# Performance work log

Measured on AMD Instinct MI355X. Metric: run time of the kernel, lower is better.

The kernel has to match this reference:

```python
import jax, jax.numpy as jnp
import numpy as np

EMBED_DIM = 32
DELTA_V = 0.5
DELTA_D = 3.0
NUM_LABELS = 20  # instance labels are 1..NUM_LABELS; 0 is background


def _safe_sqrt(x):
    # sqrt with zero-safe gradient (matches norm of identical points -> 0)
    s = jnp.where(x > 0, x, 1.0)
    return jnp.where(x > 0, jnp.sqrt(s), 0.0)


def _per_batch(emb, seg):
    # emb: [D, N], seg: [N] int labels in 0..L (0 = background)
    D, N = emb.shape
    L = NUM_LABELS
    dt = emb.dtype
    ones = jnp.ones((N,), dt)
    counts = jax.ops.segment_sum(ones, seg, num_segments=L + 1)          # [L+1]
    sums = jax.ops.segment_sum(emb.T, seg, num_segments=L + 1)          # [L+1, D]
    means = sums / jnp.maximum(counts, 1.0)[:, None]                     # [L+1, D]
    present = (counts > 0).at[0].set(False)                              # [L+1]
    num_lanes = jnp.sum(present.astype(dt))

    # --- variance (pull) loss: each pixel vs its own instance centroid ---
    mpix = means[seg]                                                    # [N, D] gather
    sq = jnp.sum((emb.T - mpix) ** 2, axis=1)                            # [N]
    d = _safe_sqrt(sq)
    v = jnp.maximum(d - DELTA_V, 0.0) ** 2 * (seg > 0).astype(dt)        # background excluded
    vsum = jax.ops.segment_sum(v, seg, num_segments=L + 1)               # [L+1]
    vmean = vsum / jnp.maximum(counts, 1.0)
    var_loss = jnp.sum(vmean * present.astype(dt)) / jnp.maximum(num_lanes, 1.0)
    var_loss = jnp.where(num_lanes > 0, var_loss, jnp.zeros((), dt))

    # --- distance (push) loss between present centroids ---
    m = means[1:]                                                        # [L, D]
    p = present[1:]                                                      # [L]
    sqd = jnp.sum((m[:, None, :] - m[None, :, :]) ** 2, axis=-1)         # [L, L]
    dist = _safe_sqrt(sqd)
    pair = (p[:, None] & p[None, :]) & ~jnp.eye(L, dtype=bool)
    dl = jnp.sum(jnp.maximum(DELTA_D - dist, 0.0) ** 2 * pair.astype(dt))
    denom = jnp.maximum(num_lanes * (num_lanes - 1.0), 1.0)
    dist_loss = jnp.where(num_lanes > 1, dl / denom / 2.0, jnp.zeros((), dt))
    return var_loss, dist_loss


def setup_inputs() -> dict:
    key = jax.random.key(0)
    k1, k2 = jax.random.split(key)
    B, D, N = 8, EMBED_DIM, 65536  # 256x256 BEV raster flattened
    embedding = jax.random.normal(k1, (B, D, N), dtype=jnp.float32)
    seg_gt = jax.random.randint(k2, (B, N), 0, NUM_LABELS + 1, dtype=jnp.int32)
    return {"embedding": embedding, "seg_gt": seg_gt}


def reference(embedding, seg_gt):
    var_b, dist_b = jax.vmap(_per_batch)(embedding, seg_gt)  # [B], [B]
    var_loss = jnp.mean(var_b)
    dist_loss = jnp.mean(dist_b)
    reg_loss = jnp.zeros((), embedding.dtype)
    return (var_loss, dist_loss, reg_loss)
```

## Files before the change

### kernel.cpp

```cpp
#include <hip/hip_runtime.h>
#include <hip/hip_cooperative_groups.h>
namespace cg = cooperative_groups;

#define NSEG 21
#define NLBL 20
#define DIM  32
#define NS   64
#define NREP 16
#define DV   0.5f
#define DD   3.0f
#define BATCH 8
#define N_PIX 65536
#define SMS  36
#define TILE_B 65536
#define SEGT_B 1024
#define DYNB  (TILE_B + SEGT_B)

using short8 = __attribute__((ext_vector_type(8))) short;
using f32x4  = __attribute__((ext_vector_type(4))) float;

#define P_OFF  0
#define C2_OFF (BATCH*DIM*NLBL*NS)
#define M_OFF  (C2_OFF + BATCH*NLBL*NS)
#define CN_OFF (M_OFF + BATCH*NLBL*DIM)
#define VS_OFF (CN_OFF + BATCH*NLBL)
#define BAR_OFF (VS_OFF + 8*BATCH*NLBL)
#define V_OFF  (BAR_OFF + 8)
#define PB_OFF (V_OFF + BATCH*NLBL*NS)

__device__ __forceinline__ short bf16rne(float f) {
  const unsigned u = __builtin_bit_cast(unsigned, f);
  return (short)((u + 0x7FFFu + ((u >> 16) & 1u)) >> 16);
}

__device__ __forceinline__ void momentsBody(const float* __restrict__ emb,
                                            const int* __restrict__ seg,
                                            float* __restrict__ ws,
                                            float* lred, ushort* tile,
                                            unsigned char* segt,
                                            int bx, int b, int tid) {
  const int wv = tid >> 6, lane = tid & 63;
  const int lr = lane & 15, lg = lane >> 4;
  const float* rowA0 = emb + ((size_t)b * DIM + lr) * N_PIX;
  const float* rowA1 = rowA0 + (size_t)16 * N_PIX;
  const int*   segb  = seg + (size_t)b * N_PIX;

  f32x4 s00 = {0,0,0,0}, s01 = {0,0,0,0}, s10 = {0,0,0,0}, s11 = {0,0,0,0};
  f32x4 c0  = {0,0,0,0}, c1  = {0,0,0,0};
  short8 ones;
  #pragma unroll
  for (int j = 0; j < 8; ++j) ones[j] = (short)0x3F80;

  #pragma unroll 2
  for (int t = 0; t < 8; ++t) {
    const int kl = wv * 256 + t * 32 + lg * 8;
    const int koff = bx * 1024 + kl;
    const float4 a00 = *(const float4*)(rowA0 + koff);
    const float4 a01 = *(const float4*)(rowA0 + koff + 4);
    const float4 a10 = *(const float4*)(rowA1 + koff);
    const float4 a11 = *(const float4*)(rowA1 + koff + 4);
    const int4   g0  = *(const int4*)(segb + koff);
    const int4   g1  = *(const int4*)(segb + koff + 4);

    short8 fa0, fa1, fb0, fb1;
    fa0[0] = bf16rne(a00.x); fa0[1] = bf16rne(a00.y);
    fa0[2] = bf16rne(a00.z); fa0[3] = bf16rne(a00.w);
    fa0[4] = bf16rne(a01.x); fa0[5] = bf16rne(a01.y);
    fa0[6] = bf16rne(a01.z); fa0[7] = bf16rne(a01.w);
    fa1[0] = bf16rne(a10.x); fa1[1] = bf16rne(a10.y);
    fa1[2] = bf16rne(a10.z); fa1[3] = bf16rne(a10.w);
    fa1[4] = bf16rne(a11.x); fa1[5] = bf16rne(a11.y);
    fa1[6] = bf16rne(a11.z); fa1[7] = bf16rne(a11.w);
    const int lab0 = lr + 1, lab1 = lr + 17;
    fb0[0] = (g0.x == lab0) ? (short)0x3F80 : (short)0;
    fb0[1] = (g0.y == lab0) ? (short)0x3F80 : (short)0;
    fb0[2] = (g0.z == lab0) ? (short)0x3F80 : (short)0;
    fb0[3] = (g0.w == lab0) ? (short)0x3F80 : (short)0;
    fb0[4] = (g1.x == lab0) ? (short)0x3F80 : (short)0;
    fb0[5] = (g1.y == lab0) ? (short)0x3F80 : (short)0;
    fb0[6] = (g1.z == lab0) ? (short)0x3F80 : (short)0;
    fb0[7] = (g1.w == lab0) ? (short)0x3F80 : (short)0;
    fb1[0] = (g0.x == lab1) ? (short)0x3F80 : (short)0;
    fb1[1] = (g0.y == lab1) ? (short)0x3F80 : (short)0;
    fb1[2] = (g0.z == lab1) ? (short)0x3F80 : (short)0;
    fb1[3] = (g0.w == lab1) ? (short)0x3F80 : (short)0;
    fb1[4] = (g1.x == lab1) ? (short)0x3F80 : (short)0;
    fb1[5] = (g1.y == lab1) ? (short)0x3F80 : (short)0;
    fb1[6] = (g1.z == lab1) ? (short)0x3F80 : (short)0;
    fb1[7] = (g1.w == lab1) ? (short)0x3F80 : (short)0;

    const int o = kl >> 3, om = o & 7;
    *(short8*)&tile[o * 256 + ((lr ^ om) << 3)] = fa0;
    *(short8*)&tile[o * 256 + (((lr ^ om) + 16) << 3)] = fa1;
    if (lr == 0) {
      unsigned long long pk =
          (unsigned long long)(g0.x & 255)        | ((unsigned long long)(g0.y & 255) << 8) |
          ((unsigned long long)(g0.z & 255) << 16) | ((unsigned long long)(g0.w & 255) << 24) |
          ((unsigned long long)(g1.x & 255) << 32) | ((unsigned long long)(g1.y & 255) << 40) |
          ((unsigned long long)(g1.z & 255) << 48) | ((unsigned long long)(g1.w & 255) << 56);
      *(unsigned long long*)&segt[o * 8] = pk;
    }

    s00 = __builtin_amdgcn_mfma_f32_16x16x32_bf16(fa0, fb0, s00, 0, 0, 0);
    s01 = __builtin_amdgcn_mfma_f32_16x16x32_bf16(fa0, fb1, s01, 0, 0, 0);
    s10 = __builtin_amdgcn_mfma_f32_16x16x32_bf16(fa1, fb0, s10, 0, 0, 0);
    s11 = __builtin_amdgcn_mfma_f32_16x16x32_bf16(fa1, fb1, s11, 0, 0, 0);
    c0  = __builtin_amdgcn_mfma_f32_16x16x32_bf16(ones, fb0, c0, 0, 0, 0);
    c1  = __builtin_amdgcn_mfma_f32_16x16x32_bf16(ones, fb1, c1, 0, 0, 0);
  }

  float vals[24];
  #pragma unroll
  for (int r = 0; r < 4; ++r) {
    vals[0 * 4 + r] = s00[r]; vals[1 * 4 + r] = s01[r];
    vals[2 * 4 + r] = s10[r]; vals[3 * 4 + r] = s11[r];
    vals[4 * 4 + r] = c0[r];  vals[5 * 4 + r] = c1[r];
  }
  #pragma unroll
  for (int w = 0; w < 4; ++w) {
    if (wv == w) {
      float* base = lred + lane * 4;
      if (w == 0) {
        #pragma unroll
        for (int f = 0; f < 6; ++f)
          #pragma unroll
          for (int r = 0; r < 4; ++r) base[f * 256 + r] = vals[f * 4 + r];
      } else {
        #pragma unroll
        for (int f = 0; f < 6; ++f)
          #pragma unroll
          for (int r = 0; r < 4; ++r) base[f * 256 + r] += vals[f * 4 + r];
      }
    }
    __syncthreads();
  }
  for (int i = tid; i < 1536; i += 256) {
    const float v = lred[i];
    const int f = i >> 8, ln = (i >> 2) & 63, r = i & 3;
    const int col = ln & 15, row = ((ln >> 4) << 2) | r;
    if (f < 4) {
      const int d = (f >> 1) * 16 + row;
      const int lcol = (f & 1) * 16 + col;
      if (lcol < NLBL)
        ws[P_OFF + (((size_t)(b * DIM + d) * NLBL) + lcol) * NS + bx] = v;
    } else {
      const int lcol = (f & 1) * 16 + col;
      if (row == 0 && lcol < NLBL)
        ws[C2_OFF + ((size_t)b * NLBL + lcol) * NS + bx] = v;
    }
  }
}

__device__ __forceinline__ void meansBody(float* __restrict__ ws, float* s_c,
                                          int bx8, int b, int tid) {
  if (tid < NLBL) {
    const float4* cp = (const float4*)(ws + C2_OFF + ((size_t)b * NLBL + tid) * NS);
    float q0 = 0.f, q1 = 0.f, q2 = 0.f, q3 = 0.f;
    #pragma unroll
    for (int k = 0; k < NS / 4; k += 4) {
      const float4 v0 = cp[k], v1 = cp[k + 1], v2 = cp[k + 2], v3 = cp[k + 3];
      q0 += v0.x + v0.y + v0.z + v0.w;
      q1 += v1.x + v1.y + v1.z + v1.w;
      q2 += v2.x + v2.y + v2.z + v2.w;
      q3 += v3.x + v3.y + v3.z + v3.w;
    }
    const float c = q0 + q1 + q2 + q3;
    if (bx8 == 0) ws[CN_OFF + b * NLBL + tid] = c;
    s_c[tid] = fmaxf(c, 1.f);
  }
  __syncthreads();
  if (tid < 80) {
    const int m = bx8 * 80 + tid;
    const int l = m >> 5, d = m & 31;
    const float4* pp = (const float4*)(ws + P_OFF + (((size_t)(b * DIM + d) * NLBL) + l) * NS);
    float q0 = 0.f, q1 = 0.f, q2 = 0.f, q3 = 0.f;
    #pragma unroll
    for (int k = 0; k < NS / 4; k += 4) {
      const float4 v0 = pp[k], v1 = pp[k + 1], v2 = pp[k + 2], v3 = pp[k + 3];
      q0 += v0.x + v0.y + v0.z + v0.w;
      q1 += v1.x + v1.y + v1.z + v1.w;
      q2 += v2.x + v2.y + v2.z + v2.w;
      q3 += v3.x + v3.y + v3.z + v3.w;
    }
    ws[M_OFF + (size_t)b * NLBL * DIM + m] = (q0 + q1 + q2 + q3) / s_c[l];
  }
}

__device__ __forceinline__ void loadMeans(const float* __restrict__ ws,
                                          float* s_m, int b, int tid) {
  for (int i = tid; i < NSEG * SMS; i += 256) s_m[i] = 0.f;
  __syncthreads();
  if (tid < 160) {
    const float4 v = ((const float4*)(ws + M_OFF + (size_t)b * NLBL * DIM))[tid];
    const int flat = tid * 4, l = flat >> 5, d = flat & 31;
    float* dst = &s_m[(l + 1) * SMS + d];
    dst[0] = v.x; dst[1] = v.y; dst[2] = v.z; dst[3] = v.w;
  }
}

__device__ __forceinline__ void varTileCompute(const ushort* tile,
                                               const unsigned char* segt,
                                               const float* s_m, float* s_v,
                                               int tid) {
  const int px0 = tid * 4;
  const int o = px0 >> 3, om = o & 7, p8 = px0 & 7;
  const int la0 = segt[px0], la1 = segt[px0 + 1], la2 = segt[px0 + 2], la3 = segt[px0 + 3];
  float q0 = 0.f, q1 = 0.f, q2 = 0.f, q3 = 0.f;
  #pragma unroll
  for (int db = 0; db < 8; ++db) {
    const f32x4 m0 = *(const f32x4*)&s_m[la0 * SMS + db * 4];
    const f32x4 m1 = *(const f32x4*)&s_m[la1 * SMS + db * 4];
    const f32x4 m2 = *(const f32x4*)&s_m[la2 * SMS + db * 4];
    const f32x4 m3 = *(const f32x4*)&s_m[la3 * SMS + db * 4];
    #pragma unroll
    for (int dd = 0; dd < 4; ++dd) {
      const int d = db * 4 + dd;
      const ushort4 ev = *(const ushort4*)&tile[o * 256 + ((d ^ om) << 3) + p8];
      float t;
      t = __builtin_bit_cast(float, (unsigned)ev.x << 16) - m0[dd]; q0 += t * t;
      t = __builtin_bit_cast(float, (unsigned)ev.y << 16) - m1[dd]; q1 += t * t;
      t = __builtin_bit_cast(float, (unsigned)ev.z << 16) - m2[dd]; q2 += t * t;
      t = __builtin_bit_cast(float, (unsigned)ev.w << 16) - m3[dd]; q3 += t * t;
    }
  }
  const int rb = (tid & (NREP - 1)) * NSEG;
  if (la0 > 0) { const float r = sqrtf(q0) - DV; if (r > 0.f) atomicAdd(&s_v[rb + la0], r * r); }
  if (la1 > 0) { const float r = sqrtf(q1) - DV; if (r > 0.f) atomicAdd(&s_v[rb + la1], r * r); }
  if (la2 > 0) { const float r = sqrtf(q2) - DV; if (r > 0.f) atomicAdd(&s_v[rb + la2], r * r); }
  if (la3 > 0) { const float r = sqrtf(q3) - DV; if (r > 0.f) atomicAdd(&s_v[rb + la3], r * r); }
}

__global__ __launch_bounds__(256, 2)
void k_fused(const float* __restrict__ emb, const int* __restrict__ seg,
             float* __restrict__ ws, float* __restrict__ out) {
  extern __shared__ __align__(16) char dynls[];
  ushort* tile = (ushort*)dynls;
  unsigned char* segt = (unsigned char*)(dynls + TILE_B);
  __shared__ __align__(16) float lred[1536];
  __shared__ __align__(16) float s_m[NSEG * SMS];
  __shared__ float s_v[NREP * NSEG];
  __shared__ float s_c[NLBL];
  __shared__ float s_vs[NLBL];
  __shared__ int   s_p[NLBL];
  __shared__ float s_red[4];
  __shared__ int   s_last;
  cg::grid_group gg = cg::this_grid();
  const int tid = threadIdx.x, bx = blockIdx.x, b = blockIdx.y;
  const int wv = tid >> 6, lane = tid & 63;

  if (bx < 8 && tid < NLBL)
    ws[VS_OFF + ((size_t)bx * BATCH + b) * NLBL + tid] = 0.f;
  if (bx == 8 && tid == 0) ((unsigned*)(ws + BAR_OFF))[b] = 0u;
  if (bx == 9 && b == 0 && tid < 3) out[tid] = 0.f;

  momentsBody(emb, seg, ws, lred, tile, segt, bx, b, tid);
  gg.sync();

  if (bx < 8) meansBody(ws, s_c, bx, b, tid);
  gg.sync();

  for (int i = tid; i < NREP * NSEG; i += 256) s_v[i] = 0.f;
  loadMeans(ws, s_m, b, tid);
  __syncthreads();
  varTileCompute(tile, segt, s_m, s_v, tid);
  __syncthreads();
  if (tid < NLBL) {
    float v = 0.f;
    #pragma unroll
    for (int r = 0; r < NREP; ++r) v += s_v[r * NSEG + (tid + 1)];
    atomicAdd(&ws[VS_OFF + ((size_t)(bx & 7) * BATCH + b) * NLBL + tid], v);
  }
  __syncthreads();
  if (tid == 0) {
    __threadfence();
    unsigned* ctr = (unsigned*)(ws + BAR_OFF);
    s_last = (atomicAdd(&ctr[b], 1u) == NS - 1) ? 1 : 0;
  }
  __syncthreads();

  if (s_last) {
    __threadfence();
    if (tid < 160) {
      const int g = tid >> 3, j = tid & 7;
      float s = atomicAdd(&ws[VS_OFF + ((size_t)j * BATCH + b) * NLBL + g], 0.f);
      s += __shfl_xor(s, 1, 64); s += __shfl_xor(s, 2, 64); s += __shfl_xor(s, 4, 64);
      if (j == 0) s_vs[g] = s;
    }
    if (tid < NLBL) {
      const float c = ws[CN_OFF + b * NLBL + tid];
      s_c[tid] = c;
      s_p[tid] = (c > 0.f) ? 1 : 0;
    }
    __syncthreads();
    float dl = 0.f;
    for (int p = tid; p < NLBL * NLBL; p += 256) {
      const int i = p / NLBL, j = p - (p / NLBL) * NLBL;
      if (i != j && s_p[i] && s_p[j]) {
        float sq = 0.f;
        #pragma unroll
        for (int d = 0; d < DIM; ++d) {
          const float t = s_m[(i + 1) * SMS + d] - s_m[(j + 1) * SMS + d];
          sq += t * t;
        }
        const float r = DD - sqrtf(sq);
        if (r > 0.f) dl += r * r;
      }
    }
    #pragma unroll
    for (int off = 32; off; off >>= 1) dl += __shfl_xor(dl, off, 64);
    if (lane == 0) s_red[wv] = dl;
    __syncthreads();
    if (tid == 0) {
      const float dsum = s_red[0] + s_red[1] + s_red[2] + s_red[3];
      float nl = 0.f, var = 0.f;
      for (int l = 0; l < NLBL; ++l)
        if (s_p[l]) { nl += 1.f; var += s_vs[l] / s_c[l]; }
      const float vb  = (nl > 0.f) ? var / nl : 0.f;
      const float db_ = (nl > 1.f) ? dsum / fmaxf(nl * (nl - 1.f), 1.f) * 0.5f : 0.f;
      atomicAdd(&out[0], vb * (1.f / BATCH));
      atomicAdd(&out[1], db_ * (1.f / BATCH));
    }
  }
}

__global__ __launch_bounds__(256)
void k_moments(const float* __restrict__ emb, const int* __restrict__ seg,
               float* __restrict__ ws) {
  extern __shared__ __align__(16) char dynls[];
  ushort* tile = (ushort*)dynls;
  unsigned char* segt = (unsigned char*)(dynls + TILE_B);
  __shared__ __align__(16) float lred[1536];
  momentsBody(emb, seg, ws, lred, tile, segt, blockIdx.x, blockIdx.y, threadIdx.x);
}
__global__ __launch_bounds__(256)
void k_means(float* __restrict__ ws) {
  __shared__ float s_c[NLBL];
  meansBody(ws, s_c, blockIdx.x, blockIdx.y, threadIdx.x);
}
__global__ __launch_bounds__(256)
void k_varG(const float* __restrict__ emb, const int* __restrict__ seg,
            float* __restrict__ ws) {
  __shared__ __align__(16) float s_m[NSEG * SMS];
  __shared__ float s_v[NREP * NSEG];
  const int tid = threadIdx.x, bx = blockIdx.x, b = blockIdx.y;
  for (int i = tid; i < NREP * NSEG; i += 256) s_v[i] = 0.f;
  loadMeans(ws, s_m, b, tid);
  __syncthreads();
  const int n0 = bx * 1024 + tid * 4;
  const int4 sl = *(const int4*)(seg + (size_t)b * N_PIX + n0);
  const float4* e4 = (const float4*)(emb + (size_t)b * DIM * N_PIX + n0);
  float q0 = 0.f, q1 = 0.f, q2 = 0.f, q3 = 0.f;
  #pragma unroll 8
  for (int d = 0; d < DIM; ++d) {
    const float4 e = e4[d * (N_PIX / 4)];
    float t;
    t = e.x - s_m[sl.x * SMS + d]; q0 += t * t;
    t = e.y - s_m[sl.y * SMS + d]; q1 += t * t;
    t = e.z - s_m[sl.z * SMS + d]; q2 += t * t;
    t = e.w - s_m[sl.w * SMS + d]; q3 += t * t;
  }
  const int rb = (tid & (NREP - 1)) * NSEG;
  if (sl.x > 0) { const float r = sqrtf(q0) - DV; if (r > 0.f) atomicAdd(&s_v[rb + sl.x], r * r); }
  if (sl.y > 0) { const float r = sqrtf(q1) - DV; if (r > 0.f) atomicAdd(&s_v[rb + sl.y], r * r); }
  if (sl.z > 0) { const float r = sqrtf(q2) - DV; if (r > 0.f) atomicAdd(&s_v[rb + sl.z], r * r); }
  if (sl.w > 0) { const float r = sqrtf(q3) - DV; if (r > 0.f) atomicAdd(&s_v[rb + sl.w], r * r); }
  __syncthreads();
  if (tid < NLBL) {
    float v = 0.f;
    #pragma unroll
    for (int r = 0; r < NREP; ++r) v += s_v[r * NSEG + (tid + 1)];
    ws[V_OFF + ((size_t)b * NLBL + tid) * NS + bx] = v;
  }
}
__global__ __launch_bounds__(256)
void k_final(float* __restrict__ ws) {
  __shared__ __align__(16) float s_m[NSEG * SMS];
  __shared__ float s_c[NLBL];
  __shared__ float s_vs[NLBL];
  __shared__ int   s_p[NLBL];
  __shared__ float s_red[4];
  const int b = blockIdx.x, tid = threadIdx.x;
  const int wv = tid >> 6, lane = tid & 63;
  loadMeans(ws, s_m, b, tid);
  __syncthreads();
  if (tid < 160) {
    const int g = tid >> 3, j = tid & 7;
    const float4* v4 = (const float4*)(ws + V_OFF + ((size_t)b * NLBL + g) * NS + j * 8);
    const float4 a = v4[0], c = v4[1];
    float s = a.x + a.y + a.z + a.w + c.x + c.y + c.z + c.w;
    s += __shfl_xor(s, 1, 64); s += __shfl_xor(s, 2, 64); s += __shfl_xor(s, 4, 64);
    if (j == 0) s_vs[g] = s;
  }
  if (tid < NLBL) {
    const float c = ws[CN_OFF + b * NLBL + tid];
    s_c[tid] = c;
    s_p[tid] = (c > 0.f) ? 1 : 0;
  }
  __syncthreads();
  float dl = 0.f;
  for (int p = tid; p < NLBL * NLBL; p += 256) {
    const int i = p / NLBL, j = p - (p / NLBL) * NLBL;
    if (i != j && s_p[i] && s_p[j]) {
      float sq = 0.f;
      #pragma unroll
      for (int d = 0; d < DIM; ++d) {
        const float t = s_m[(i + 1) * SMS + d] - s_m[(j + 1) * SMS + d];
        sq += t * t;
      }
      const float r = DD - sqrtf(sq);
      if (r > 0.f) dl += r * r;
    }
  }
  #pragma unroll
  for (int off = 32; off; off >>= 1) dl += __shfl_xor(dl, off, 64);
  if (lane == 0) s_red[wv] = dl;
  __syncthreads();
  if (tid == 0) {
    const float dsum = s_red[0] + s_red[1] + s_red[2] + s_red[3];
    float nl = 0.f, var = 0.f;
    for (int l = 0; l < NLBL; ++l)
      if (s_p[l]) { nl += 1.f; var += s_vs[l] / s_c[l]; }
    ws[PB_OFF + b * 2]     = (nl > 0.f) ? var / nl : 0.f;
    ws[PB_OFF + b * 2 + 1] = (nl > 1.f) ? dsum / fmaxf(nl * (nl - 1.f), 1.f) * 0.5f : 0.f;
  }
}
__global__ __launch_bounds__(64)
void k_out(const float* __restrict__ ws, float* __restrict__ out) {
  const int tid = threadIdx.x;
  float v = 0.f, d = 0.f;
  if (tid < BATCH) {
    v = ws[PB_OFF + tid * 2];
    d = ws[PB_OFF + tid * 2 + 1];
  }
  #pragma unroll
  for (int off = 4; off; off >>= 1) { v += __shfl_xor(v, off, 64); d += __shfl_xor(d, off, 64); }
  if (tid == 0) {
    out[0] = v / (float)BATCH;
    out[1] = d / (float)BATCH;
    out[2] = 0.f;
  }
}

extern "C" void kernel_launch(void* const* d_in, const int* in_sizes, int n_in,
                              void* d_out, int out_size, void* d_ws, size_t ws_size,
                              hipStream_t stream) {
  const float* emb = (const float*)d_in[0];
  const int*   seg = (const int*)d_in[1];
  float* out = (float*)d_out;
  float* ws  = (float*)d_ws;

  int maxB = 0;
  bool coop = false;
  if (hipOccupancyMaxActiveBlocksPerMultiprocessor(&maxB, (const void*)k_fused, 256, DYNB)
        == hipSuccess)
    coop = ((long)maxB * 256 >= (long)NS * BATCH);
  if (coop) {
    void* args[] = {(void*)&emb, (void*)&seg, (void*)&ws, (void*)&out};
    if (hipLaunchCooperativeKernel((const void*)k_fused, dim3(NS, BATCH), dim3(256),
                                   args, DYNB, stream) == hipSuccess)
      return;
  }
  k_moments<<<dim3(NS, BATCH), 256, DYNB, stream>>>(emb, seg, ws);
  k_means  <<<dim3(8, BATCH), 256, 0, stream>>>(ws);
  k_varG   <<<dim3(NS, BATCH), 256, 0, stream>>>(emb, seg, ws);
  k_final  <<<dim3(BATCH), 256, 0, stream>>>(ws);
  k_out    <<<1, 64, 0, stream>>>(ws, out);
}
```

Before: 42.59 us.

## Stage embedding tile into LDS with coalesced loads before MFMA moment pass

The moment pass now loads embedding and labels in a separate cooperative phase. Each thread reads float4 along the pixel axis for all 32 dims, converts to bf16 and writes swizzled LDS, and packs the labels into a byte table. After a barrier, the MFMA loop reads its A fragments and labels from LDS instead of global memory. This replaces the old per-lane strided global loads with fully coalesced streaming, at the cost of an extra barrier and extra LDS traffic.

```diff
diff --git a/kernel.cpp b/kernel.cpp
--- a/kernel.cpp
+++ b/kernel.cpp
@@ -28,9 +28,9 @@
 #define V_OFF  (BAR_OFF + 8)
 #define PB_OFF (V_OFF + BATCH*NLBL*NS)
 
-__device__ __forceinline__ short bf16rne(float f) {
+__device__ __forceinline__ ushort bf16rne(float f) {
   const unsigned u = __builtin_bit_cast(unsigned, f);
-  return (short)((u + 0x7FFFu + ((u >> 16) & 1u)) >> 16);
+  return (ushort)((u + 0x7FFFu + ((u >> 16) & 1u)) >> 16);
 }
 
 __device__ __forceinline__ void momentsBody(const float* __restrict__ emb,
@@ -41,64 +41,57 @@
                                             int bx, int b, int tid) {
   const int wv = tid >> 6, lane = tid & 63;
   const int lr = lane & 15, lg = lane >> 4;
-  const float* rowA0 = emb + ((size_t)b * DIM + lr) * N_PIX;
-  const float* rowA1 = rowA0 + (size_t)16 * N_PIX;
-  const int*   segb  = seg + (size_t)b * N_PIX;
+  const int base = bx * 1024;
+
+  {
+    const int4 g = *(const int4*)(seg + (size_t)b * N_PIX + base + tid * 4);
+    const unsigned pk = (unsigned)(g.x & 255) | ((unsigned)(g.y & 255) << 8) |
+                        ((unsigned)(g.z & 255) << 16) | ((unsigned)(g.w & 255) << 24);
+    *(unsigned*)&segt[tid * 4] = pk;
+
+    const int o1 = tid >> 1, om1 = o1 & 7;
+    const int sub = (tid & 1) * 4;
+    const float* ebase = emb + (size_t)b * DIM * N_PIX + base + tid * 4;
+    #pragma unroll 4
+    for (int d = 0; d < DIM; ++d) {
+      const float4 e = *(const float4*)(ebase + (size_t)d * N_PIX);
+      const ushort r0 = bf16rne(e.x), r1 = bf16rne(e.y);
+      const ushort r2 = bf16rne(e.z), r3 = bf16rne(e.w);
+      uint2 w;
+      w.x = (unsigned)r0 | ((unsigned)r1 << 16);
+      w.y = (unsigned)r2 | ((unsigned)r3 << 16);
+      *(uint2*)&tile[o1 * 256 + ((d ^ om1) << 3) + sub] = w;
+    }
+  }
+  __syncthreads();
 
   f32x4 s00 = {0,0,0,0}, s01 = {0,0,0,0}, s10 = {0,0,0,0}, s11 = {0,0,0,0};
   f32x4 c0  = {0,0,0,0}, c1  = {0,0,0,0};
   short8 ones;
   #pragma unroll
   for (int j = 0; j < 8; ++j) ones[j] = (short)0x3F80;
+  const int lab0 = lr + 1, lab1 = lr + 17;
 
   #pragma unroll 2
   for (int t = 0; t < 8; ++t) {
     const int kl = wv * 256 + t * 32 + lg * 8;
-    const int koff = bx * 1024 + kl;
-    const float4 a00 = *(const float4*)(rowA0 + koff);
-    const float4 a01 = *(const float4*)(rowA0 + koff + 4);
-    const float4 a10 = *(const float4*)(rowA1 + koff);
-    const float4 a11 = *(const float4*)(rowA1 + koff + 4);
-    const int4   g0  = *(const int4*)(segb + koff);
-    const int4   g1  = *(const int4*)(segb + koff + 4);
-
-    short8 fa0, fa1, fb0, fb1;
-    fa0[0] = bf16rne(a00.x); fa0[1] = bf16rne(a00.y);
-    fa0[2] = bf16rne(a00.z); fa0[3] = bf16rne(a00.w);
-    fa0[4] = bf16rne(a01.x); fa0[5] = bf16rne(a01.y);
-    fa0[6] = bf16rne(a01.z); fa0[7] = bf16rne(a01.w);
-    fa1[0] = bf16rne(a10.x); fa1[1] = bf16rne(a10.y);
-    fa1[2] = bf16rne(a10.z); fa1[3] = bf16rne(a10.w);
-    fa1[4] = bf16rne(a11.x); fa1[5] = bf16rne(a11.y);
-    fa1[6] = bf16rne(a11.z); fa1[7] = bf16rne(a11.w);
-    const int lab0 = lr + 1, lab1 = lr + 17;
-    fb0[0] = (g0.x == lab0) ? (short)0x3F80 : (short)0;
-    fb0[1] = (g0.y == lab0) ? (short)0x3F80 : (short)0;
-    fb0[2] = (g0.z == lab0) ? (short)0x3F80 : (short)0;
-    fb0[3] = (g0.w == lab0) ? (short)0x3F80 : (short)0;
-    fb0[4] = (g1.x == lab0) ? (short)0x3F80 : (short)0;
-    fb0[5] = (g1.y == lab0) ? (short)0x3F80 : (short)0;
-    fb0[6] = (g1.z == lab0) ? (short)0x3F80 : (short)0;
-    fb0[7] = (g1.w == lab0) ? (short)0x3F80 : (short)0;
-    fb1[0] = (g0.x == lab1) ? (short)0x3F80 : (short)0;
-    fb1[1] = (g0.y == lab1) ? (short)0x3F80 : (short)0;
-    fb1[2] = (g0.z == lab1) ? (short)0x3F80 : (short)0;
-    fb1[3] = (g0.w == lab1) ? (short)0x3F80 : (short)0;
-    fb1[4] = (g1.x == lab1) ? (short)0x3F80 : (short)0;
-    fb1[5] = (g1.y == lab1) ? (short)0x3F80 : (short)0;
-    fb1[6] = (g1.z == lab1) ? (short)0x3F80 : (short)0;
-    fb1[7] = (g1.w == lab1) ? (short)0x3F80 : (short)0;
-
     const int o = kl >> 3, om = o & 7;
-    *(short8*)&tile[o * 256 + ((lr ^ om) << 3)] = fa0;
-    *(short8*)&tile[o * 256 + (((lr ^ om) + 16) << 3)] = fa1;
-    if (lr == 0) {
-      unsigned long long pk =
-          (unsigned long long)(g0.x & 255)        | ((unsigned long long)(g0.y & 255) << 8) |
-          ((unsigned long long)(g0.z & 255) << 16) | ((unsigned long long)(g0.w & 255) << 24) |
-          ((unsigned long long)(g1.x & 255) << 32) | ((unsigned long long)(g1.y & 255) << 40) |
-          ((unsigned long long)(g1.z & 255) << 48) | ((unsigned long long)(g1.w & 255) << 56);
-      *(unsigned long long*)&segt[o * 8] = pk;
+    const short8 fa0 = *(const short8*)&tile[o * 256 + ((lr ^ om) << 3)];
+    const short8 fa1 = *(const short8*)&tile[o * 256 + (((lr ^ om) + 16) << 3)];
+    const uint2 gp = *(const uint2*)&segt[kl];
+
+    short8 fb0, fb1;
+    #pragma unroll
+    for (int j = 0; j < 4; ++j) {
+      const int bj = (int)((gp.x >> (8 * j)) & 255u);
+      fb0[j] = (bj == lab0) ? (short)0x3F80 : (short)0;
+      fb1[j] = (bj == lab1) ? (short)0x3F80 : (short)0;
+    }
+    #pragma unroll
+    for (int j = 0; j < 4; ++j) {
+      const int bj = (int)((gp.y >> (8 * j)) & 255u);
+      fb0[4 + j] = (bj == lab0) ? (short)0x3F80 : (short)0;
+      fb1[4 + j] = (bj == lab1) ? (short)0x3F80 : (short)0;
     }
 
     s00 = __builtin_amdgcn_mfma_f32_16x16x32_bf16(fa0, fb0, s00, 0, 0, 0);
@@ -119,17 +112,17 @@
   #pragma unroll
   for (int w = 0; w < 4; ++w) {
     if (wv == w) {
-      float* base = lred + lane * 4;
+      float* basep = lred + lane * 4;
       if (w == 0) {
         #pragma unroll
         for (int f = 0; f < 6; ++f)
           #pragma unroll
-          for (int r = 0; r < 4; ++r) base[f * 256 + r] = vals[f * 4 + r];
+          for (int r = 0; r < 4; ++r) basep[f * 256 + r] = vals[f * 4 + r];
       } else {
         #pragma unroll
         for (int f = 0; f < 6; ++f)
           #pragma unroll
-          for (int r = 0; r < 4; ++r) base[f * 256 + r] += vals[f * 4 + r];
+          for (int r = 0; r < 4; ++r) basep[f * 256 + r] += vals[f * 4 + r];
       }
     }
     __syncthreads();
```

Result: slower. 48.02 us (+12.7%).
